# Performance work log

Hardware: AMD Instinct MI355X
Metric: run time of the kernel (lower is better)

## Reference

```python
import jax, jax.numpy as jnp
import numpy as np

HIDDEN = 1024
HEADS = 16
HEAD_DIM = HIDDEN // HEADS


def setup_inputs() -> dict:
    key = jax.random.key(0)
    ks = jax.random.split(key, 11)
    s = 1.0 / np.sqrt(HIDDEN)
    return {
        "query": jax.random.normal(ks[0], (8, 1024, HIDDEN), dtype=jnp.float32),
        "key": jax.random.normal(ks[1], (8, 1024, HIDDEN), dtype=jnp.float32),
        "value": jax.random.normal(ks[2], (8, 1024, HIDDEN), dtype=jnp.float32),
        "Wq": jax.random.uniform(ks[3], (HIDDEN, HIDDEN), jnp.float32, -s, s),
        "bq": jax.random.uniform(ks[4], (HIDDEN,), jnp.float32, -s, s),
        "Wk": jax.random.uniform(ks[5], (HIDDEN, HIDDEN), jnp.float32, -s, s),
        "bk": jax.random.uniform(ks[6], (HIDDEN,), jnp.float32, -s, s),
        "Wv": jax.random.uniform(ks[7], (HIDDEN, HIDDEN), jnp.float32, -s, s),
        "bv": jax.random.uniform(ks[8], (HIDDEN,), jnp.float32, -s, s),
        "Wo": jax.random.uniform(ks[9], (HIDDEN, HIDDEN), jnp.float32, -s, s),
        "bo": jax.random.uniform(ks[10], (HIDDEN,), jnp.float32, -s, s),
    }


def reference(query, key, value, Wq, bq, Wk, bk, Wv, bv, Wo, bo):
    B, S, D = key.shape
    scale = jnp.sqrt(jnp.asarray(HEAD_DIM, dtype=query.dtype))
    # linear projections (torch Linear: x @ W.T + b), split into heads -> [B,H,S,hd]
    def proj(x, W, b):
        return (x @ W.T + b).reshape(B, -1, HEADS, HEAD_DIM).transpose(0, 2, 1, 3)
    q = proj(query, Wq, bq)
    k = proj(key, Wk, bk)
    v = proj(value, Wv, bv)
    # [B,H,Sq,Sk] full attention scores (module materializes them)
    energy = jnp.einsum("bhqd,bhkd->bhqk", q, k) / scale
    attention = jax.nn.softmax(energy, axis=-1)
    # dropout p=0.0 -> identity
    x = jnp.einsum("bhqk,bhkd->bhqd", attention, v)
    x = x.transpose(0, 2, 1, 3).reshape(B, -1, D)
    return x @ Wo.T + bo
```

## Files before the change

### kernel.cpp

```cpp
#include <hip/hip_runtime.h>
#include <hip/hip_bf16.h>
#include <stdint.h>

#define HIDDEN 1024
#define HEADS 16
#define HD 64
#define BATCH 8
#define SEQ 1024
#define MTOT (BATCH*SEQ)

typedef __attribute__((ext_vector_type(4))) float  f32x4;
typedef __attribute__((ext_vector_type(4))) float  float4v;
typedef __attribute__((ext_vector_type(8))) short  s16x8;
typedef __attribute__((ext_vector_type(4))) short  s16x4;
typedef __attribute__((ext_vector_type(4))) unsigned int u32x4;
typedef __bf16 bf16x8 __attribute__((ext_vector_type(8)));

#define QSCALE 0.18033688011112042f

__device__ __forceinline__ short f2bf(float f) {
  uint32_t u = __builtin_bit_cast(uint32_t, f);
  u += 0x7FFFu + ((u >> 16) & 1u);
  return (short)(u >> 16);
}
__device__ __forceinline__ bf16x8 asbf(s16x8 v) {
  return __builtin_bit_cast(bf16x8, v);
}

__device__ __forceinline__ float dpp_fmax16(float x) {
  int t;
  t = __builtin_amdgcn_update_dpp(0, __builtin_bit_cast(int, x), 0xB1, 0xF, 0xF, true);
  x = fmaxf(x, __builtin_bit_cast(float, t));
  t = __builtin_amdgcn_update_dpp(0, __builtin_bit_cast(int, x), 0x4E, 0xF, 0xF, true);
  x = fmaxf(x, __builtin_bit_cast(float, t));
  t = __builtin_amdgcn_update_dpp(0, __builtin_bit_cast(int, x), 0x141, 0xF, 0xF, true);
  x = fmaxf(x, __builtin_bit_cast(float, t));
  t = __builtin_amdgcn_update_dpp(0, __builtin_bit_cast(int, x), 0x140, 0xF, 0xF, true);
  x = fmaxf(x, __builtin_bit_cast(float, t));
  return x;
}
__device__ __forceinline__ float dpp_fadd16(float x) {
  int t;
  t = __builtin_amdgcn_update_dpp(0, __builtin_bit_cast(int, x), 0xB1, 0xF, 0xF, true);
  x += __builtin_bit_cast(float, t);
  t = __builtin_amdgcn_update_dpp(0, __builtin_bit_cast(int, x), 0x4E, 0xF, 0xF, true);
  x += __builtin_bit_cast(float, t);
  t = __builtin_amdgcn_update_dpp(0, __builtin_bit_cast(int, x), 0x141, 0xF, 0xF, true);
  x += __builtin_bit_cast(float, t);
  t = __builtin_amdgcn_update_dpp(0, __builtin_bit_cast(int, x), 0x140, 0xF, 0xF, true);
  x += __builtin_bit_cast(float, t);
  return x;
}

typedef const __attribute__((address_space(1))) void* gvp;
typedef __attribute__((address_space(3)))       void* lvp;
__device__ __forceinline__ void gl_lds16(const void* g, const void* ldsbase) {
  __builtin_amdgcn_global_load_lds((gvp)(uintptr_t)g,
                                   (lvp)(uintptr_t)(uint32_t)(uintptr_t)ldsbase,
                                   16, 0, 0);
}

__global__ __launch_bounds__(256) void cvt_x(const float* __restrict__ src,
                                             short* __restrict__ dst) {
  int i = blockIdx.x * 256 + threadIdx.x;
  float4v a = *(const float4v*)(src + (size_t)i * 8);
  float4v b = *(const float4v*)(src + (size_t)i * 8 + 4);
  s16x8 o = { f2bf(a.x), f2bf(a.y), f2bf(a.z), f2bf(a.w),
              f2bf(b.x), f2bf(b.y), f2bf(b.z), f2bf(b.w) };
  *(s16x8*)(dst + (size_t)i * 8) = o;
}

__global__ __launch_bounds__(256) void cvt_x3(const float* __restrict__ s0,
                                              const float* __restrict__ s1,
                                              const float* __restrict__ s2,
                                              short* __restrict__ dst) {
  int z = blockIdx.y;
  const float* src = (z == 0) ? s0 : (z == 1) ? s1 : s2;
  int i = blockIdx.x * 256 + threadIdx.x;
  float4v a = *(const float4v*)(src + (size_t)i * 8);
  float4v b = *(const float4v*)(src + (size_t)i * 8 + 4);
  s16x8 o = { f2bf(a.x), f2bf(a.y), f2bf(a.z), f2bf(a.w),
              f2bf(b.x), f2bf(b.y), f2bf(b.z), f2bf(b.w) };
  *(s16x8*)(dst + (size_t)z * ((size_t)MTOT * 1024) + (size_t)i * 8) = o;
}

__global__ __launch_bounds__(256) void cvt_w(const float* __restrict__ s0,
                                             const float* __restrict__ s1,
                                             const float* __restrict__ s2,
                                             const float* __restrict__ s3,
                                             short* __restrict__ dst) {
  int z = blockIdx.y;
  const float* src = (z == 0) ? s0 : (z == 1) ? s1 : (z == 2) ? s2 : s3;
  int i = blockIdx.x * 256 + threadIdx.x;
  float4v a = *(const float4v*)(src + (size_t)i * 8);
  float4v b = *(const float4v*)(src + (size_t)i * 8 + 4);
  s16x8 o = { f2bf(a.x), f2bf(a.y), f2bf(a.z), f2bf(a.w),
              f2bf(b.x), f2bf(b.y), f2bf(b.z), f2bf(b.w) };
  *(s16x8*)(dst + (size_t)z * 1048576 + (size_t)i * 8) = o;
}

__global__ __launch_bounds__(256) void vtrans(const short* __restrict__ Vb,
                                              short* __restrict__ Vt) {
  __shared__ short lt[64 * 64];
  const int t = threadIdx.x;
  const int kt0 = blockIdx.x, h = blockIdx.y, b = blockIdx.z;
  const short* src = Vb + ((size_t)(b * 1024 + kt0 * 64)) * 1024 + h * 64;

  #pragma unroll
  for (int i = 0; i < 2; i++) {
    int c = t + i * 256;
    int s = c >> 3, dc = c & 7;
    s16x8 v = *(const s16x8*)(src + (size_t)s * 1024 + dc * 8);
    int dcp = dc ^ (s & 7) ^ ((s >> 3) & 7);
    *(s16x8*)(&lt[s * 64 + dcp * 8]) = v;
  }
  __syncthreads();

  short* dst = Vt + ((size_t)(b * 16 + h) * 64) * 1024 + kt0 * 64;
  #pragma unroll
  for (int i = 0; i < 2; i++) {
    int c = t + i * 256;
    int d = c >> 3, kc = c & 7;
    s16x8 o;
    #pragma unroll
    for (int j = 0; j < 8; j++) {
      int s = kc * 8 + j;
      o[j] = lt[s * 64 + (((d >> 3) ^ j ^ kc) * 8) + (d & 7)];
    }
    *(s16x8*)(dst + (size_t)d * 1024 + (kc ^ (d & 7)) * 8) = o;
  }
}

template<int CMODE>
__global__ __launch_bounds__(256, 2) void gemm_bf16_dma(
    const short* __restrict__ A, const short* __restrict__ Wb,
    const float* __restrict__ bias, void* __restrict__ Cv, float scale)
{
  __shared__ short Alds[128 * 32];
  __shared__ short Blds[128 * 32];

  const int t  = threadIdx.x;
  const int w  = t >> 6, l = t & 63, g = l >> 4, ln = l & 15;
  const int wr = w >> 1, wc = w & 1;
  const int m0 = blockIdx.x * 128, n0 = blockIdx.y * 128;

  f32x4 acc[4][4];
  #pragma unroll
  for (int i = 0; i < 4; i++)
    #pragma unroll
    for (int j = 0; j < 4; j++) acc[i][j] = (f32x4)0.0f;

  for (int k0 = 0; k0 < 1024; k0 += 32) {
    #pragma unroll
    for (int i = 0; i < 2; i++) {
      int c = i * 256 + w * 64 + l;
      int row = c >> 2, col8 = c & 3;
      gl_lds16(A  + (size_t)(m0 + row) * 1024 + k0 + col8 * 8,
               &Alds[(i * 256 + w * 64) * 8]);
      gl_lds16(Wb + (size_t)(n0 + row) * 1024 + k0 + col8 * 8,
               &Blds[(i * 256 + w * 64) * 8]);
    }
    __syncthreads();

    s16x8 af[4], bfr[4];
    #pragma unroll
    for (int mf = 0; mf < 4; mf++)
      af[mf] = *(const s16x8*)(&Alds[(wr * 64 + mf * 16 + ln) * 32 + g * 8]);
    #pragma unroll
    for (int nf = 0; nf < 4; nf++)
      bfr[nf] = *(const s16x8*)(&Blds[(wc * 64 + nf * 16 + ln) * 32 + g * 8]);

    __builtin_amdgcn_s_setprio(1);
    #pragma unroll
    for (int mf = 0; mf < 4; mf++)
      #pragma unroll
      for (int nf = 0; nf < 4; nf++)
        acc[mf][nf] = __builtin_amdgcn_mfma_f32_16x16x32_bf16(
            asbf(af[mf]), asbf(bfr[nf]), acc[mf][nf], 0, 0, 0);
    __builtin_amdgcn_s_setprio(0);
    __syncthreads();
  }

  float bv[4];
  #pragma unroll
  for (int nf = 0; nf < 4; nf++) bv[nf] = bias[n0 + wc * 64 + nf * 16 + ln];
  #pragma unroll
  for (int mf = 0; mf < 4; mf++)
    #pragma unroll
    for (int nf = 0; nf < 4; nf++)
      #pragma unroll
      for (int r = 0; r < 4; r++) {
        float vv = (acc[mf][nf][r] + bv[nf]) * scale;
        size_t idx = (size_t)(m0 + wr * 64 + mf * 16 + g * 4 + r) * 1024
                   + n0 + wc * 64 + nf * 16 + ln;
        if constexpr (CMODE == 0) ((float*)Cv)[idx] = vv;
        else if constexpr (CMODE == 1) ((short*)Cv)[idx] = f2bf(vv);
        else {
          size_t idxs = idx ^ (size_t)(((g * 4 + r) & 7) * 8);
          ((short*)Cv)[idxs] = f2bf(vv);
        }
      }
}

__global__ __launch_bounds__(256, 2) void gemm_qkv(
    const short* __restrict__ X3, const short* __restrict__ Wb,
    const float* __restrict__ bq, const float* __restrict__ bk,
    const float* __restrict__ bv_, short* __restrict__ Qb,
    short* __restrict__ Kb, short* __restrict__ Vb)
{
  __shared__ short Alds[128 * 32];
  __shared__ short Blds[128 * 32];

  const size_t E = (size_t)MTOT * 1024;
  const int z = blockIdx.z;
  const short* A  = X3 + (size_t)z * E;
  const short* W  = Wb + (size_t)z * 1048576;
  const float* bias = (z == 0) ? bq : (z == 1) ? bk : bv_;
  short* Cv = (z == 0) ? Qb : (z == 1) ? Kb : Vb;
  const float scale = (z == 0) ? QSCALE : 1.0f;
  const bool kswz = (z == 1);

  const int t  = threadIdx.x;
  const int w  = t >> 6, l = t & 63, g = l >> 4, ln = l & 15;
  const int wr = w >> 1, wc = w & 1;
  const int m0 = blockIdx.x * 128, n0 = blockIdx.y * 128;

  f32x4 acc[4][4];
  #pragma unroll
  for (int i = 0; i < 4; i++)
    #pragma unroll
    for (int j = 0; j < 4; j++) acc[i][j] = (f32x4)0.0f;

  for (int k0 = 0; k0 < 1024; k0 += 32) {
    #pragma unroll
    for (int i = 0; i < 2; i++) {
      int c = i * 256 + w * 64 + l;
      int row = c >> 2, col8 = c & 3;
      gl_lds16(A + (size_t)(m0 + row) * 1024 + k0 + col8 * 8,
               &Alds[(i * 256 + w * 64) * 8]);
      gl_lds16(W + (size_t)(n0 + row) * 1024 + k0 + col8 * 8,
               &Blds[(i * 256 + w * 64) * 8]);
    }
    __syncthreads();

    s16x8 af[4], bfr[4];
    #pragma unroll
    for (int mf = 0; mf < 4; mf++)
      af[mf] = *(const s16x8*)(&Alds[(wr * 64 + mf * 16 + ln) * 32 + g * 8]);
    #pragma unroll
    for (int nf = 0; nf < 4; nf++)
      bfr[nf] = *(const s16x8*)(&Blds[(wc * 64 + nf * 16 + ln) * 32 + g * 8]);

    __builtin_amdgcn_s_setprio(1);
    #pragma unroll
    for (int mf = 0; mf < 4; mf++)
      #pragma unroll
      for (int nf = 0; nf < 4; nf++)
        acc[mf][nf] = __builtin_amdgcn_mfma_f32_16x16x32_bf16(
            asbf(af[mf]), asbf(bfr[nf]), acc[mf][nf], 0, 0, 0);
    __builtin_amdgcn_s_setprio(0);
    __syncthreads();
  }

  float bv[4];
  #pragma unroll
  for (int nf = 0; nf < 4; nf++) bv[nf] = bias[n0 + wc * 64 + nf * 16 + ln];
  #pragma unroll
  for (int mf = 0; mf < 4; mf++)
    #pragma unroll
    for (int nf = 0; nf < 4; nf++)
      #pragma unroll
      for (int r = 0; r < 4; r++) {
        float vv = (acc[mf][nf][r] + bv[nf]) * scale;
        size_t idx = (size_t)(m0 + wr * 64 + mf * 16 + g * 4 + r) * 1024
                   + n0 + wc * 64 + nf * 16 + ln;
        if (kswz) idx ^= (size_t)(((g * 4 + r) & 7) * 8);
        Cv[idx] = f2bf(vv);
      }
}

template<bool A_IS_BF16, bool OUT_IS_F32>
__global__ __launch_bounds__(256, 2) void gemm_bt_bias(
    const void* __restrict__ Av, const float* __restrict__ W,
    const float* __restrict__ bias, void* __restrict__ Cv, float scale)
{
  __shared__ short Alds[128 * 32];
  __shared__ short Blds[128 * 32];

  const int t  = threadIdx.x;
  const int w  = t >> 6, l = t & 63, g = l >> 4, ln = l & 15;
  const int wr = w >> 1, wc = w & 1;
  const int m0 = blockIdx.x * 128, n0 = blockIdx.y * 128;

  f32x4 acc[4][4];
  #pragma unroll
  for (int i = 0; i < 4; i++)
    #pragma unroll
    for (int j = 0; j < 4; j++) acc[i][j] = (f32x4)0.0f;

  const float* Af = (const float*)Av;
  const short* Ab = (const short*)Av;

  for (int k0 = 0; k0 < 1024; k0 += 32) {
    if constexpr (!A_IS_BF16) {
      #pragma unroll
      for (int i = 0; i < 4; i++) {
        int c = i * 256 + t;
        int row = c >> 3, c4 = c & 7;
        float4v v = *(const float4v*)(Af + (size_t)(m0 + row) * 1024 + k0 + c4 * 4);
        s16x4 p = { f2bf(v.x), f2bf(v.y), f2bf(v.z), f2bf(v.w) };
        *(s16x4*)(&Alds[row * 32 + c4 * 4]) = p;
      }
    } else {
      #pragma unroll
      for (int i = 0; i < 2; i++) {
        int c = i * 256 + t;
        int row = c >> 2, c8 = c & 3;
        *(s16x8*)(&Alds[row * 32 + c8 * 8]) =
            *(const s16x8*)(Ab + (size_t)(m0 + row) * 1024 + k0 + c8 * 8);
      }
    }
    #pragma unroll
    for (int i = 0; i < 4; i++) {
      int c = i * 256 + t;
      int row = c >> 3, c4 = c & 7;
      float4v v = *(const float4v*)(W + (size_t)(n0 + row) * 1024 + k0 + c4 * 4);
      s16x4 p = { f2bf(v.x), f2bf(v.y), f2bf(v.z), f2bf(v.w) };
      *(s16x4*)(&Blds[row * 32 + c4 * 4]) = p;
    }
    __syncthreads();

    s16x8 af[4], bfr[4];
    #pragma unroll
    for (int mf = 0; mf < 4; mf++)
      af[mf] = *(const s16x8*)(&Alds[(wr * 64 + mf * 16 + ln) * 32 + g * 8]);
    #pragma unroll
    for (int nf = 0; nf < 4; nf++)
      bfr[nf] = *(const s16x8*)(&Blds[(wc * 64 + nf * 16 + ln) * 32 + g * 8]);

    #pragma unroll
    for (int mf = 0; mf < 4; mf++)
      #pragma unroll
      for (int nf = 0; nf < 4; nf++)
        acc[mf][nf] = __builtin_amdgcn_mfma_f32_16x16x32_bf16(
            asbf(af[mf]), asbf(bfr[nf]), acc[mf][nf], 0, 0, 0);
    __syncthreads();
  }

  float bv[4];
  #pragma unroll
  for (int nf = 0; nf < 4; nf++) bv[nf] = bias[n0 + wc * 64 + nf * 16 + ln];
  #pragma unroll
  for (int mf = 0; mf < 4; mf++)
    #pragma unroll
    for (int nf = 0; nf < 4; nf++)
      #pragma unroll
      for (int r = 0; r < 4; r++) {
        float vv = (acc[mf][nf][r] + bv[nf]) * scale;
        size_t idx = (size_t)(m0 + wr * 64 + mf * 16 + g * 4 + r) * 1024
                   + n0 + wc * 64 + nf * 16 + ln;
        if constexpr (OUT_IS_F32) ((float*)Cv)[idx] = vv;
        else                      ((short*)Cv)[idx] = f2bf(vv);
      }
}

__global__ __launch_bounds__(256, 2) void flash_attn(
    const short* __restrict__ Q, const short* __restrict__ Kswz,
    const short* __restrict__ Vt, short* __restrict__ CTX)
{
  __shared__ short Klds[2][64 * 64];
  __shared__ short Vlds[2][64 * 64];

  const int t  = threadIdx.x;
  const int w  = t >> 6, l = t & 63, g = l >> 4, ln = l & 15;
  const int rb0 = g & 1, rb1 = g >> 1;
  const bool sendK = (rb0 ^ rb1) != 0;
  const int bh   = blockIdx.x & 127;
  const int tile = blockIdx.x >> 7;
  const int b = bh >> 4, h = bh & 15;
  const size_t rowbase = (size_t)b * SEQ;
  const int colbase = h * HD;
  const int q0w = tile * 128 + w * 32;

  const short* Kg = Kswz + rowbase * 1024 + colbase;
  const short* Vg = Vt + (size_t)bh * 65536;
  const int c0 = w * 64 + l;

  const short one_bf = (short)0x3F80;
  const s16x8 ones = { one_bf, one_bf, one_bf, one_bf,
                       one_bf, one_bf, one_bf, one_bf };

  s16x8 qf[2][2];
  #pragma unroll
  for (int mf = 0; mf < 2; mf++)
    #pragma unroll
    for (int kf = 0; kf < 2; kf++)
      qf[mf][kf] = *(const s16x8*)(Q + (rowbase + q0w + mf * 16 + ln) * 1024
                                     + colbase + kf * 32 + g * 8);

  f32x4 acc_o[2][4];
  f32x4 l_acc[2];
  #pragma unroll
  for (int i = 0; i < 2; i++) {
    l_acc[i] = (f32x4)0.0f;
    #pragma unroll
    for (int j = 0; j < 4; j++) acc_o[i][j] = (f32x4)0.0f;
  }

  float m_run[2] = { -1e30f, -1e30f };

  auto STAGE = [&](int buf, int nt) {
    #pragma unroll
    for (int i = 0; i < 2; i++) {
      int c = c0 + i * 256;
      gl_lds16(Kg + (size_t)(nt * 64 + (c >> 3)) * 1024 + (c & 7) * 8,
               &Klds[buf][(i * 256 + w * 64) * 8]);
      gl_lds16(Vg + (size_t)(c >> 3) * 1024 + nt * 64 + (c & 7) * 8,
               &Vlds[buf][(i * 256 + w * 64) * 8]);
    }
  };

  STAGE(0, 0);
  __syncthreads();

  int cur = 0;
  for (int kt = 0; kt < 16; kt++) {
    if (kt < 15) STAGE(cur ^ 1, kt + 1);

    const short* Kc = &Klds[cur][0];
    const short* Vc = &Vlds[cur][0];

    f32x4 sT[4][2];
    #pragma unroll
    for (int i = 0; i < 4; i++)
      #pragma unroll
      for (int j = 0; j < 2; j++) sT[i][j] = (f32x4)0.0f;

    __builtin_amdgcn_s_setprio(1);
    #pragma unroll
    for (int kf = 0; kf < 2; kf++) {
      s16x8 kfr[4];
      #pragma unroll
      for (int nf = 0; nf < 4; nf++)
        kfr[nf] = *(const s16x8*)(Kc + (nf * 16 + ln) * 64
                                     + (((kf * 4 + g) ^ (ln & 7)) * 8));
      #pragma unroll
      for (int kk4 = 0; kk4 < 4; kk4++)
        #pragma unroll
        for (int kq = 0; kq < 2; kq++)
          sT[kk4][kq] = __builtin_amdgcn_mfma_f32_16x16x32_bf16(
              asbf(kfr[kk4]), asbf(qf[kq][kf]), sT[kk4][kq], 0, 0, 0);
    }
    __builtin_amdgcn_s_setprio(0);

    float rm[2];
    #pragma unroll
    for (int kq = 0; kq < 2; kq++) {
      float a0 = fmaxf(sT[0][kq][0], sT[0][kq][1]);
      float a1 = fmaxf(sT[0][kq][2], sT[0][kq][3]);
      float a2 = fmaxf(sT[1][kq][0], sT[1][kq][1]);
      float a3 = fmaxf(sT[1][kq][2], sT[1][kq][3]);
      float a4 = fmaxf(sT[2][kq][0], sT[2][kq][1]);
      float a5 = fmaxf(sT[2][kq][2], sT[2][kq][3]);
      float a6 = fmaxf(sT[3][kq][0], sT[3][kq][1]);
      float a7 = fmaxf(sT[3][kq][2], sT[3][kq][3]);
      float b0 = fmaxf(a0, a1), b1 = fmaxf(a2, a3);
      float b2 = fmaxf(a4, a5), b3 = fmaxf(a6, a7);
      float mx = fmaxf(fmaxf(b0, b1), fmaxf(b2, b3));
      mx = fmaxf(mx, __shfl_xor(mx, 16));
      mx = fmaxf(mx, __shfl_xor(mx, 32));
      rm[kq] = mx;
    }
    float worst = fmaxf(rm[0] - m_run[0], rm[1] - m_run[1]);

    if (__all(worst <= 8.0f)) {
      #pragma unroll
      for (int kq = 0; kq < 2; kq++) {
        float m0v = m_run[kq];
        #pragma unroll
        for (int kk4 = 0; kk4 < 4; kk4++)
          #pragma unroll
          for (int r = 0; r < 4; r++)
            sT[kk4][kq][r] = exp2f(sT[kk4][kq][r] - m0v);
      }
    } else {
      float sc[2];
      #pragma unroll
      for (int kq = 0; kq < 2; kq++) {
        float mnew = fmaxf(m_run[kq], rm[kq]);
        sc[kq] = exp2f(m_run[kq] - mnew);
        m_run[kq] = mnew;
        #pragma unroll
        for (int kk4 = 0; kk4 < 4; kk4++)
          #pragma unroll
          for (int r = 0; r < 4; r++)
            sT[kk4][kq][r] = exp2f(sT[kk4][kq][r] - mnew);
      }
      #pragma unroll
      for (int mf = 0; mf < 2; mf++)
        #pragma unroll
        for (int r = 0; r < 4; r++) {
          float scr = __shfl(sc[mf], g * 4 + r);
          l_acc[mf][r] *= scr;
          #pragma unroll
          for (int nf = 0; nf < 4; nf++) acc_o[mf][nf][r] *= scr;
        }
    }

    uint32_t D[4][2][2];
    #pragma unroll
    for (int kk4 = 0; kk4 < 4; kk4++)
      #pragma unroll
      for (int kq = 0; kq < 2; kq++) {
        asm("v_cvt_pk_bf16_f32 %0, %1, %2"
            : "=v"(D[kk4][kq][0]) : "v"(sT[kk4][kq][0]), "v"(sT[kk4][kq][1]));
        asm("v_cvt_pk_bf16_f32 %0, %1, %2"
            : "=v"(D[kk4][kq][1]) : "v"(sT[kk4][kq][2]), "v"(sT[kk4][kq][3]));
      }

    s16x8 pa[2][2];
    #pragma unroll
    for (int kq = 0; kq < 2; kq++)
      #pragma unroll
      for (int kp = 0; kp < 2; kp++) {
        uint32_t K0 = rb1 ? D[2*kp+1][kq][0] : D[2*kp][kq][0];
        uint32_t K1 = rb1 ? D[2*kp+1][kq][1] : D[2*kp][kq][1];
        uint32_t S0 = rb1 ? D[2*kp][kq][0]   : D[2*kp+1][kq][0];
        uint32_t S1 = rb1 ? D[2*kp][kq][1]   : D[2*kp+1][kq][1];
        uint32_t R0 = (uint32_t)__shfl_xor((int)S0, 32);
        uint32_t R1 = (uint32_t)__shfl_xor((int)S1, 32);
        uint32_t T0 = sendK ? K0 : R0, T1 = sendK ? K1 : R1;
        uint32_t V0 = sendK ? R0 : K0, V1 = sendK ? R1 : K1;
        uint32_t U0 = (uint32_t)__shfl_xor((int)T0, 16);
        uint32_t U1 = (uint32_t)__shfl_xor((int)T1, 16);
        u32x4 dw = { rb0 ? U0 : V0, rb0 ? U1 : V1,
                     rb0 ? V0 : U0, rb0 ? V1 : U1 };
        pa[kq][kp] = __builtin_bit_cast(s16x8, dw);
      }

    s16x8 vbf[4][2];
    #pragma unroll
    for (int nf = 0; nf < 4; nf++)
      #pragma unroll
      for (int kf = 0; kf < 2; kf++)
        vbf[nf][kf] = *(const s16x8*)(Vc + (nf * 16 + ln) * 64
                                         + (((kf * 4 + g) ^ (ln & 7)) * 8));

    __builtin_amdgcn_s_setprio(1);
    #pragma unroll
    for (int kf = 0; kf < 2; kf++)
      #pragma unroll
      for (int mf = 0; mf < 2; mf++) {
        l_acc[mf] = __builtin_amdgcn_mfma_f32_16x16x32_bf16(
            asbf(pa[mf][kf]), asbf(ones), l_acc[mf], 0, 0, 0);
        #pragma unroll
        for (int nf = 0; nf < 4; nf++)
          acc_o[mf][nf] = __builtin_amdgcn_mfma_f32_16x16x32_bf16(
              asbf(pa[mf][kf]), asbf(vbf[nf][kf]), acc_o[mf][nf], 0, 0, 0);
      }
    __builtin_amdgcn_s_setprio(0);

    __syncthreads();
    cur ^= 1;
  }

  #pragma unroll
  for (int mf = 0; mf < 2; mf++)
    #pragma unroll
    for (int r = 0; r < 4; r++) {
      float inv = 1.0f / l_acc[mf][r];
      size_t row = rowbase + q0w + mf * 16 + g * 4 + r;
      #pragma unroll
      for (int nf = 0; nf < 4; nf++)
        CTX[row * 1024 + colbase + nf * 16 + ln] = f2bf(acc_o[mf][nf][r] * inv);
    }
}

__global__ __launch_bounds__(256, 2) void flash_attn_fb(
    const short* __restrict__ Q, const short* __restrict__ K,
    const short* __restrict__ V, short* __restrict__ CTX)
{
  __shared__ short Klds[2][64 * 64];
  __shared__ short Vtl [2][64 * 64];
  __shared__ short Plds[4][32 * 72];

  const int t  = threadIdx.x;
  const int w  = t >> 6, l = t & 63, g = l >> 4, ln = l & 15;
  const int tile = blockIdx.x & 7;
  const int bh   = blockIdx.x >> 3;
  const int b = bh >> 4, h = bh & 15;
  const size_t rowbase = (size_t)b * SEQ;
  const int colbase = h * HD;
  const int q0w = tile * 128 + w * 32;

  const int kk0  = t >> 3;
  const int dblk = t & 7;
  const int ksw  = (dblk ^ (kk0 & 7)) * 8;
  const int kWr  = kk0 * 64 + dblk * 8;
  const short* Kg = K + rowbase * 1024 + colbase + ksw;
  const short* Vg = V + rowbase * 1024 + colbase + dblk * 8;

  s16x8 qf[2][2];
  #pragma unroll
  for (int mf = 0; mf < 2; mf++)
    #pragma unroll
    for (int kf = 0; kf < 2; kf++)
      qf[mf][kf] = *(const s16x8*)(Q + (rowbase + q0w + mf * 16 + ln) * 1024
                                     + colbase + kf * 32 + g * 8);

  f32x4 acc_o[2][4];
  #pragma unroll
  for (int i = 0; i < 2; i++)
    #pragma unroll
    for (int j = 0; j < 4; j++) acc_o[i][j] = (f32x4)0.0f;

  float m_run[2][4], l_run[2][4];
  #pragma unroll
  for (int i = 0; i < 2; i++)
    #pragma unroll
    for (int r = 0; r < 4; r++) { m_run[i][r] = -1e30f; l_run[i][r] = 0.0f; }

  auto storeKV = [&](int buf, s16x8 ka, s16x8 kb, s16x8 va, s16x8 vb8) {
    short* Kd = &Klds[buf][0];
    short* Vd = &Vtl[buf][0];
    *(s16x8*)(Kd + kWr)        = ka;
    *(s16x8*)(Kd + kWr + 2048) = kb;
    #pragma unroll
    for (int e = 0; e < 8; e++) {
      int a0 = (dblk * 8 + e) * 64 + (kk0 ^ ((e ^ dblk) * 8));
      Vd[a0]      = va[e];
      Vd[a0 ^ 32] = vb8[e];
    }
  };

  s16x8 kvA = *(const s16x8*)(Kg + (size_t)kk0 * 1024);
  s16x8 kvB = *(const s16x8*)(Kg + (size_t)(kk0 + 32) * 1024);
  s16x8 vvA = *(const s16x8*)(Vg + (size_t)kk0 * 1024);
  s16x8 vvB = *(const s16x8*)(Vg + (size_t)(kk0 + 32) * 1024);
  storeKV(0, kvA, kvB, vvA, vvB);

  int cur = 0;
  for (int kt = 0; kt < 16; kt++) {
    if (kt < 15) {
      const size_t r0 = (size_t)((kt + 1) * 64 + kk0) * 1024;
      kvA = *(const s16x8*)(Kg + r0);
      kvB = *(const s16x8*)(Kg + r0 + 32 * 1024);
      vvA = *(const s16x8*)(Vg + r0);
      vvB = *(const s16x8*)(Vg + r0 + 32 * 1024);
    }
    __syncthreads();

    const short* Kc = &Klds[cur][0];
    const short* Vc = &Vtl[cur][0];

    f32x4 s_acc[2][4];
    #pragma unroll
    for (int i = 0; i < 2; i++)
      #pragma unroll
      for (int j = 0; j < 4; j++) s_acc[i][j] = (f32x4)0.0f;

    #pragma unroll
    for (int kf = 0; kf < 2; kf++) {
      s16x8 kfr[4];
      #pragma unroll
      for (int nf = 0; nf < 4; nf++)
        kfr[nf] = *(const s16x8*)(Kc + (nf * 16 + ln) * 64
                                     + (((kf * 4 + g) ^ (ln & 7)) * 8));
      #pragma unroll
      for (int mf = 0; mf < 2; mf++)
        #pragma unroll
        for (int nf = 0; nf < 4; nf++)
          s_acc[mf][nf] = __builtin_amdgcn_mfma_f32_16x16x32_bf16(
              asbf(qf[mf][kf]), asbf(kfr[nf]), s_acc[mf][nf], 0, 0, 0);
    }

    float smax[2][4];
    float worst = -1e30f;
    #pragma unroll
    for (int mf = 0; mf < 2; mf++)
      #pragma unroll
      for (int r = 0; r < 4; r++) {
        float mx = fmaxf(fmaxf(s_acc[mf][0][r], s_acc[mf][1][r]),
                         fmaxf(s_acc[mf][2][r], s_acc[mf][3][r]));
        mx = dpp_fmax16(mx);
        smax[mf][r] = mx;
        worst = fmaxf(worst, mx - m_run[mf][r]);
      }

    if (__all(worst <= 8.0f)) {
      #pragma unroll
      for (int mf = 0; mf < 2; mf++)
        #pragma unroll
        for (int r = 0; r < 4; r++) {
          float m0v = m_run[mf][r];
          float rs = 0.0f;
          #pragma unroll
          for (int nf = 0; nf < 4; nf++) {
            float pv = exp2f(s_acc[mf][nf][r] - m0v);
            s_acc[mf][nf][r] = pv;
            rs += pv;
          }
          l_run[mf][r] += rs;
        }
    } else {
      #pragma unroll
      for (int mf = 0; mf < 2; mf++)
        #pragma unroll
        for (int r = 0; r < 4; r++) {
          float mnew = fmaxf(m_run[mf][r], smax[mf][r]);
          float sc = exp2f(m_run[mf][r] - mnew);
          m_run[mf][r] = mnew;
          float rs = 0.0f;
          #pragma unroll
          for (int nf = 0; nf < 4; nf++) {
            float pv = exp2f(s_acc[mf][nf][r] - mnew);
            s_acc[mf][nf][r] = pv;
            rs += pv;
          }
          l_run[mf][r] = l_run[mf][r] * sc + rs;
          #pragma unroll
          for (int nf = 0; nf < 4; nf++) acc_o[mf][nf][r] *= sc;
        }
    }

    short* Pw = &Plds[w][0];
    #pragma unroll
    for (int mf = 0; mf < 2; mf++)
      #pragma unroll
      for (int nf = 0; nf < 4; nf++) {
        uint32_t p01, p23;
        asm("v_cvt_pk_bf16_f32 %0, %1, %2"
            : "=v"(p01) : "v"(s_acc[mf][nf][0]), "v"(s_acc[mf][nf][1]));
        asm("v_cvt_pk_bf16_f32 %0, %1, %2"
            : "=v"(p23) : "v"(s_acc[mf][nf][2]), "v"(s_acc[mf][nf][3]));
        int pb = (mf * 16 + g * 4) * 72 + ((nf * 16 + ln) ^ (g << 3));
        Pw[pb]       = (short)p01;
        Pw[pb + 72]  = (short)(p01 >> 16);
        Pw[pb + 144] = (short)p23;
        Pw[pb + 216] = (short)(p23 >> 16);
      }

    s16x8 pa[2][2], vbf[4][2];
    #pragma unroll
    for (int mf = 0; mf < 2; mf++)
      #pragma unroll
      for (int kf = 0; kf < 2; kf++)
        pa[mf][kf] = *(const s16x8*)(
            &Pw[(mf * 16 + ln) * 72 + (((kf * 4 + g) ^ (ln >> 2)) << 3)]);
    #pragma unroll
    for (int nf = 0; nf < 4; nf++)
      #pragma unroll
      for (int kf = 0; kf < 2; kf++) {
        int d  = nf * 16 + ln;
        int sw = (d & 7) ^ (d >> 3);
        vbf[nf][kf] = *(const s16x8*)(Vc + d * 64 + ((kf * 32 + g * 8) ^ (sw * 8)));
      }

    #pragma unroll
    for (int kf = 0; kf < 2; kf++)
      #pragma unroll
      for (int mf = 0; mf < 2; mf++)
        #pragma unroll
        for (int nf = 0; nf < 4; nf++)
          acc_o[mf][nf] = __builtin_amdgcn_mfma_f32_16x16x32_bf16(
              asbf(pa[mf][kf]), asbf(vbf[nf][kf]), acc_o[mf][nf], 0, 0, 0);

    if (kt < 15) {
      storeKV(cur ^ 1, kvA, kvB, vvA, vvB);
      cur ^= 1;
    }
  }

  #pragma unroll
  for (int mf = 0; mf < 2; mf++)
    #pragma unroll
    for (int r = 0; r < 4; r++) {
      float inv = 1.0f / dpp_fadd16(l_run[mf][r]);
      size_t row = rowbase + q0w + mf * 16 + g * 4 + r;
      #pragma unroll
      for (int nf = 0; nf < 4; nf++)
        CTX[row * 1024 + colbase + nf * 16 + ln] = f2bf(acc_o[mf][nf][r] * inv);
    }
}

extern "C" void kernel_launch(void* const* d_in, const int* in_sizes, int n_in,
                              void* d_out, int out_size, void* d_ws, size_t ws_size,
                              hipStream_t stream) {
  const float* query = (const float*)d_in[0];
  const float* key   = (const float*)d_in[1];
  const float* value = (const float*)d_in[2];
  const float* Wq = (const float*)d_in[3];
  const float* bq = (const float*)d_in[4];
  const float* Wk = (const float*)d_in[5];
  const float* bk = (const float*)d_in[6];
  const float* Wv = (const float*)d_in[7];
  const float* bv = (const float*)d_in[8];
  const float* Wo = (const float*)d_in[9];
  const float* bo = (const float*)d_in[10];

  const size_t E = (size_t)MTOT * 1024;
  const size_t need_b = (7 * E + 4ull * 1048576) * 2;
  const size_t need_s = (5 * E + 4ull * 1048576) * 2;

  dim3 gg(MTOT / 128, HIDDEN / 128), bb(256);
  dim3 fg(BATCH * HEADS * (SEQ / 128));

  if (ws_size >= need_b) {
    short* Qb = (short*)d_ws;
    short* Kb = Qb + E;
    short* Vb = Kb + E;
    short* Cx = Vb + E;
    short* T0 = Cx + E;
    short* Wb = T0 + 3 * E;

    cvt_w<<<dim3(512, 4), bb, 0, stream>>>(Wq, Wk, Wv, Wo, Wb);
    cvt_x3<<<dim3(4096, 3), bb, 0, stream>>>(query, key, value, T0);
    gemm_qkv<<<dim3(MTOT / 128, HIDDEN / 128, 3), bb, 0, stream>>>(
        T0, Wb, bq, bk, bv, Qb, Kb, Vb);
    vtrans<<<dim3(16, 16, 8), bb, 0, stream>>>(Vb, T0);
    flash_attn<<<fg, bb, 0, stream>>>(Qb, Kb, T0, Cx);
    gemm_bf16_dma<0><<<gg, bb, 0, stream>>>(Cx, Wb + 3 * 1048576, bo,
                                            (float*)d_out, 1.0f);
  } else if (ws_size >= need_s) {
    short* Qb = (short*)d_ws;
    short* Kb = Qb + E;
    short* Vb = Kb + E;
    short* Cx = Vb + E;
    short* T  = Cx + E;
    short* Wb = T  + E;

    cvt_w<<<dim3(512, 4), bb, 0, stream>>>(Wq, Wk, Wv, Wo, Wb);
    cvt_x<<<4096, bb, 0, stream>>>(query, T);
    gemm_bf16_dma<1><<<gg, bb, 0, stream>>>(T, Wb + 0 * 1048576, bq, Qb, QSCALE);
    cvt_x<<<4096, bb, 0, stream>>>(key, T);
    gemm_bf16_dma<2><<<gg, bb, 0, stream>>>(T, Wb + 1 * 1048576, bk, Kb, 1.0f);
    cvt_x<<<4096, bb, 0, stream>>>(value, T);
    gemm_bf16_dma<1><<<gg, bb, 0, stream>>>(T, Wb + 2 * 1048576, bv, Vb, 1.0f);
    vtrans<<<dim3(16, 16, 8), bb, 0, stream>>>(Vb, T);
    flash_attn<<<fg, bb, 0, stream>>>(Qb, Kb, T, Cx);
    gemm_bf16_dma<0><<<gg, bb, 0, stream>>>(Cx, Wb + 3 * 1048576, bo,
                                            (float*)d_out, 1.0f);
  } else {
    short* Qb = (short*)d_ws;
    short* Kb = Qb + E;
    short* Vb = Kb + E;
    short* Cx = Vb + E;

    gemm_bt_bias<false, false><<<gg, bb, 0, stream>>>(query, Wq, bq, Qb, QSCALE);
    gemm_bt_bias<false, false><<<gg, bb, 0, stream>>>(key,   Wk, bk, Kb, 1.0f);
    gemm_bt_bias<false, false><<<gg, bb, 0, stream>>>(value, Wv, bv, Vb, 1.0f);
    flash_attn_fb<<<fg, bb, 0, stream>>>(Qb, Kb, Vb, Cx);
    gemm_bt_bias<true, true><<<gg, bb, 0, stream>>>(Cx, Wo, bo, (float*)d_out, 1.0f);
  }
}
```

Baseline: 212.5 us.

## Double GEMM K-tile to 64 with XOR-swizzled bf16 layouts for conflict-free LDS

```diff
diff --git a/kernel.cpp b/kernel.cpp
--- a/kernel.cpp
+++ b/kernel.cpp
@@ -63,11 +63,13 @@
 __global__ __launch_bounds__(256) void cvt_x(const float* __restrict__ src,
                                              short* __restrict__ dst) {
   int i = blockIdx.x * 256 + threadIdx.x;
+  int row = i >> 7, c = i & 127;
+  int group = c >> 3, sub = (c & 7) ^ (row & 7);
   float4v a = *(const float4v*)(src + (size_t)i * 8);
   float4v b = *(const float4v*)(src + (size_t)i * 8 + 4);
   s16x8 o = { f2bf(a.x), f2bf(a.y), f2bf(a.z), f2bf(a.w),
               f2bf(b.x), f2bf(b.y), f2bf(b.z), f2bf(b.w) };
-  *(s16x8*)(dst + (size_t)i * 8) = o;
+  *(s16x8*)(dst + (size_t)row * 1024 + group * 64 + sub * 8) = o;
 }
 
 __global__ __launch_bounds__(256) void cvt_x3(const float* __restrict__ s0,
@@ -77,11 +79,14 @@
   int z = blockIdx.y;
   const float* src = (z == 0) ? s0 : (z == 1) ? s1 : s2;
   int i = blockIdx.x * 256 + threadIdx.x;
+  int row = i >> 7, c = i & 127;
+  int group = c >> 3, sub = (c & 7) ^ (row & 7);
   float4v a = *(const float4v*)(src + (size_t)i * 8);
   float4v b = *(const float4v*)(src + (size_t)i * 8 + 4);
   s16x8 o = { f2bf(a.x), f2bf(a.y), f2bf(a.z), f2bf(a.w),
               f2bf(b.x), f2bf(b.y), f2bf(b.z), f2bf(b.w) };
-  *(s16x8*)(dst + (size_t)z * ((size_t)MTOT * 1024) + (size_t)i * 8) = o;
+  *(s16x8*)(dst + (size_t)z * ((size_t)MTOT * 1024)
+                + (size_t)row * 1024 + group * 64 + sub * 8) = o;
 }
 
 __global__ __launch_bounds__(256) void cvt_w(const float* __restrict__ s0,
@@ -92,11 +97,14 @@
   int z = blockIdx.y;
   const float* src = (z == 0) ? s0 : (z == 1) ? s1 : (z == 2) ? s2 : s3;
   int i = blockIdx.x * 256 + threadIdx.x;
+  int row = i >> 7, c = i & 127;
+  int group = c >> 3, sub = (c & 7) ^ (row & 7);
   float4v a = *(const float4v*)(src + (size_t)i * 8);
   float4v b = *(const float4v*)(src + (size_t)i * 8 + 4);
   s16x8 o = { f2bf(a.x), f2bf(a.y), f2bf(a.z), f2bf(a.w),
               f2bf(b.x), f2bf(b.y), f2bf(b.z), f2bf(b.w) };
-  *(s16x8*)(dst + (size_t)z * 1048576 + (size_t)i * 8) = o;
+  *(s16x8*)(dst + (size_t)z * 1048576
+                + (size_t)row * 1024 + group * 64 + sub * 8) = o;
 }
 
 __global__ __launch_bounds__(256) void vtrans(const short* __restrict__ Vb,
@@ -136,8 +144,8 @@
     const short* __restrict__ A, const short* __restrict__ Wb,
     const float* __restrict__ bias, void* __restrict__ Cv, float scale)
 {
-  __shared__ short Alds[128 * 32];
-  __shared__ short Blds[128 * 32];
+  __shared__ short Alds[128 * 64];
+  __shared__ short Blds[128 * 64];
 
   const int t  = threadIdx.x;
   const int w  = t >> 6, l = t & 63, g = l >> 4, ln = l & 15;
@@ -150,34 +158,41 @@
     #pragma unroll
     for (int j = 0; j < 4; j++) acc[i][j] = (f32x4)0.0f;
 
-  for (int k0 = 0; k0 < 1024; k0 += 32) {
-    #pragma unroll
-    for (int i = 0; i < 2; i++) {
+  for (int k0 = 0; k0 < 1024; k0 += 64) {
+    #pragma unroll
+    for (int i = 0; i < 4; i++) {
       int c = i * 256 + w * 64 + l;
-      int row = c >> 2, col8 = c & 3;
-      gl_lds16(A  + (size_t)(m0 + row) * 1024 + k0 + col8 * 8,
+      int row = c >> 3, cb = c & 7;
+      gl_lds16(A  + (size_t)(m0 + row) * 1024 + k0 + cb * 8,
                &Alds[(i * 256 + w * 64) * 8]);
-      gl_lds16(Wb + (size_t)(n0 + row) * 1024 + k0 + col8 * 8,
+      gl_lds16(Wb + (size_t)(n0 + row) * 1024 + k0 + cb * 8,
                &Blds[(i * 256 + w * 64) * 8]);
     }
     __syncthreads();
 
-    s16x8 af[4], bfr[4];
-    #pragma unroll
-    for (int mf = 0; mf < 4; mf++)
-      af[mf] = *(const s16x8*)(&Alds[(wr * 64 + mf * 16 + ln) * 32 + g * 8]);
-    #pragma unroll
-    for (int nf = 0; nf < 4; nf++)
-      bfr[nf] = *(const s16x8*)(&Blds[(wc * 64 + nf * 16 + ln) * 32 + g * 8]);
-
-    __builtin_amdgcn_s_setprio(1);
-    #pragma unroll
-    for (int mf = 0; mf < 4; mf++)
-      #pragma unroll
-      for (int nf = 0; nf < 4; nf++)
-        acc[mf][nf] = __builtin_amdgcn_mfma_f32_16x16x32_bf16(
-            asbf(af[mf]), asbf(bfr[nf]), acc[mf][nf], 0, 0, 0);
-    __builtin_amdgcn_s_setprio(0);
+    #pragma unroll
+    for (int kf = 0; kf < 2; kf++) {
+      s16x8 af[4], bfr[4];
+      #pragma unroll
+      for (int mf = 0; mf < 4; mf++) {
+        int row = wr * 64 + mf * 16 + ln;
+        af[mf] = *(const s16x8*)(&Alds[row * 64 + (((kf * 4 + g) ^ (ln & 7)) * 8)]);
+      }
+      #pragma unroll
+      for (int nf = 0; nf < 4; nf++) {
+        int row = wc * 64 + nf * 16 + ln;
+        bfr[nf] = *(const s16x8*)(&Blds[row * 64 + (((kf * 4 + g) ^ (ln & 7)) * 8)]);
+      }
+
+      __builtin_amdgcn_s_setprio(1);
+      #pragma unroll
+      for (int mf = 0; mf < 4; mf++)
+        #pragma unroll
+        for (int nf = 0; nf < 4; nf++)
+          acc[mf][nf] = __builtin_amdgcn_mfma_f32_16x16x32_bf16(
+              asbf(af[mf]), asbf(bfr[nf]), acc[mf][nf], 0, 0, 0);
+      __builtin_amdgcn_s_setprio(0);
+    }
     __syncthreads();
   }
 
@@ -208,8 +223,8 @@
     const float* __restrict__ bv_, short* __restrict__ Qb,
     short* __restrict__ Kb, short* __restrict__ Vb)
 {
-  __shared__ short Alds[128 * 32];
-  __shared__ short Blds[128 * 32];
+  __shared__ short Alds[128 * 64];
+  __shared__ short Blds[128 * 64];
 
   const size_t E = (size_t)MTOT * 1024;
   const int z = blockIdx.z;
@@ -231,34 +246,41 @@
     #pragma unroll
     for (int j = 0; j < 4; j++) acc[i][j] = (f32x4)0.0f;
 
-  for (int k0 = 0; k0 < 1024; k0 += 32) {
-    #pragma unroll
-    for (int i = 0; i < 2; i++) {
+  for (int k0 = 0; k0 < 1024; k0 += 64) {
+    #pragma unroll
+    for (int i = 0; i < 4; i++) {
       int c = i * 256 + w * 64 + l;
-      int row = c >> 2, col8 = c & 3;
-      gl_lds16(A + (size_t)(m0 + row) * 1024 + k0 + col8 * 8,
+      int row = c >> 3, cb = c & 7;
+      gl_lds16(A + (size_t)(m0 + row) * 1024 + k0 + cb * 8,
                &Alds[(i * 256 + w * 64) * 8]);
-      gl_lds16(W + (size_t)(n0 + row) * 1024 + k0 + col8 * 8,
+      gl_lds16(W + (size_t)(n0 + row) * 1024 + k0 + cb * 8,
                &Blds[(i * 256 + w * 64) * 8]);
     }
     __syncthreads();
 
-    s16x8 af[4], bfr[4];
-    #pragma unroll
-    for (int mf = 0; mf < 4; mf++)
-      af[mf] = *(const s16x8*)(&Alds[(wr * 64 + mf * 16 + ln) * 32 + g * 8]);
-    #pragma unroll
-    for (int nf = 0; nf < 4; nf++)
-      bfr[nf] = *(const s16x8*)(&Blds[(wc * 64 + nf * 16 + ln) * 32 + g * 8]);
-
-    __builtin_amdgcn_s_setprio(1);
-    #pragma unroll
-    for (int mf = 0; mf < 4; mf++)
-      #pragma unroll
-      for (int nf = 0; nf < 4; nf++)
-        acc[mf][nf] = __builtin_amdgcn_mfma_f32_16x16x32_bf16(
-            asbf(af[mf]), asbf(bfr[nf]), acc[mf][nf], 0, 0, 0);
-    __builtin_amdgcn_s_setprio(0);
+    #pragma unroll
+    for (int kf = 0; kf < 2; kf++) {
+      s16x8 af[4], bfr[4];
+      #pragma unroll
+      for (int mf = 0; mf < 4; mf++) {
+        int row = wr * 64 + mf * 16 + ln;
+        af[mf] = *(const s16x8*)(&Alds[row * 64 + (((kf * 4 + g) ^ (ln & 7)) * 8)]);
+      }
+      #pragma unroll
+      for (int nf = 0; nf < 4; nf++) {
+        int row = wc * 64 + nf * 16 + ln;
+        bfr[nf] = *(const s16x8*)(&Blds[row * 64 + (((kf * 4 + g) ^ (ln & 7)) * 8)]);
+      }
+
+      __builtin_amdgcn_s_setprio(1);
+      #pragma unroll
+      for (int mf = 0; mf < 4; mf++)
+        #pragma unroll
+        for (int nf = 0; nf < 4; nf++)
+          acc[mf][nf] = __builtin_amdgcn_mfma_f32_16x16x32_bf16(
+              asbf(af[mf]), asbf(bfr[nf]), acc[mf][nf], 0, 0, 0);
+      __builtin_amdgcn_s_setprio(0);
+    }
     __syncthreads();
   }
 
@@ -570,9 +592,14 @@
     for (int r = 0; r < 4; r++) {
       float inv = 1.0f / l_acc[mf][r];
       size_t row = rowbase + q0w + mf * 16 + g * 4 + r;
-      #pragma unroll
-      for (int nf = 0; nf < 4; nf++)
-        CTX[row * 1024 + colbase + nf * 16 + ln] = f2bf(acc_o[mf][nf][r] * inv);
+      int rs = (g * 4 + r) & 7;
+      #pragma unroll
+      for (int nf = 0; nf < 4; nf++) {
+        int tc = nf * 16 + ln;
+        int sb = (tc >> 3) ^ rs;
+        CTX[row * 1024 + colbase + sb * 8 + (tc & 7)] =
+            f2bf(acc_o[mf][nf][r] * inv);
+      }
     }
 }
 
```

New measurement: 204.3 us. 1.04x faster.
